# Performance work log

Measured on AMD Instinct MI355X. Metric: run time of the kernel, lower is better.

Reference implementation:

```python
import jax, jax.numpy as jnp
import numpy as np
import math

B, L, D = 2, 2048, 512
H, HD = 8, 64                      # num_heads, head_dim = D // H
NG = D * (D - 1) // 2              # SO(D) generator count = 130816


def setup_inputs() -> dict:
    key = jax.random.key(0)
    ks = jax.random.split(key, 8)
    x = jax.random.normal(ks[0], (B, L, D), jnp.float32)
    # additive causal mask [L, L]
    mask = jnp.where(jnp.tril(jnp.ones((L, L), bool)), 0.0, -1e9).astype(jnp.float32)
    coef = lambda k: jax.random.normal(k, (NG,), jnp.float32) * 0.1
    basis = lambda k: jax.random.normal(k, (HD, HD), jnp.float32) * 0.1
    return {
        "x": x, "mask": mask,
        "coef_q": coef(ks[1]), "coef_k": coef(ks[2]),
        "coef_v": coef(ks[3]), "coef_o": coef(ks[4]),
        "bias_q": jnp.zeros((D,), jnp.float32), "bias_k": jnp.zeros((D,), jnp.float32),
        "bias_v": jnp.zeros((D,), jnp.float32), "bias_o": jnp.zeros((D,), jnp.float32),
        "basis_q": basis(ks[5]), "basis_k": basis(ks[6]),
    }


def _make_W(coefs):
    # W = I + sum_i coef_i * G_i, with G_i the antisymmetric basis (row-major i<j).
    iu = jnp.triu_indices(D, k=1)
    A = jnp.zeros((D, D), coefs.dtype).at[iu].set(coefs)
    return A - A.T + jnp.eye(D, dtype=coefs.dtype)


def _proj(x, coefs, bias):
    # F.linear(x, W, b) = x @ W.T + b
    return x @ _make_W(coefs).T + bias


def _invariants(t, basis):
    # t: [B, H, L, HD] -> concat(norm, t @ basis.T)[..., :HD]
    norm = jnp.linalg.norm(t, axis=-1, keepdims=True)
    ip = jnp.einsum('bhld,nd->bhln', t, basis)
    return jnp.concatenate([norm, ip], axis=-1)[..., :HD]


def reference(x, mask, coef_q, coef_k, coef_v, coef_o,
              bias_q, bias_k, bias_v, bias_o, basis_q, basis_k):
    split = lambda t: t.reshape(B, L, H, HD).transpose(0, 2, 1, 3)  # [B,H,L,HD]
    Q = split(_proj(x, coef_q, bias_q))
    K = split(_proj(x, coef_k, bias_k))
    V = split(_proj(x, coef_v, bias_v))
    Qi = _invariants(Q, basis_q)
    Ki = _invariants(K, basis_k)
    scores = jnp.einsum('bhld,bhmd->bhlm', Qi, Ki) / math.sqrt(HD) + mask
    attn = jax.nn.softmax(scores, axis=-1)
    out = jnp.einsum('bhlm,bhmd->bhld', attn, V)
    out = out.transpose(0, 2, 1, 3).reshape(B, L, D)
    return _proj(out, coef_o, bias_o)
```

## Files before the change

kernel.cpp:

```cpp
#include <hip/hip_runtime.h>
#include <hip/hip_bf16.h>
#include <math.h>

#define D_ 512
#define B_ 2
#define L_ 2048
#define H_ 8
#define HD_ 64

typedef __attribute__((ext_vector_type(8))) short short8;
typedef __attribute__((ext_vector_type(4))) float f32x4;
typedef _Float16 half8 __attribute__((ext_vector_type(8)));

__device__ __forceinline__ ushort f2bf(float f) {
  __hip_bfloat16 h = __float2bfloat16(f);
  return *(ushort*)&h;
}
__device__ __forceinline__ float bf2f(ushort u) {
  unsigned int v = ((unsigned int)u) << 16;
  union { unsigned int u; float f; } c; c.u = v; return c.f;
}
__device__ __forceinline__ ushort f2h(float f) {
  _Float16 h = (_Float16)f;
  return *(ushort*)&h;
}
__device__ __forceinline__ int swz(int row, int col) {
  return row*64 + (((col>>3) ^ (row&7))<<3) + (col&7);
}
__device__ __forceinline__ int tri_idx(int i, int j) {
  return i*(D_-1) - (i*(i-1))/2 + (j - i - 1);
}

#define GLL16(g, l) __builtin_amdgcn_global_load_lds( \
    (const __attribute__((address_space(1))) void*)(g), \
    (__attribute__((address_space(3))) void*)(l), 16, 0, 0)

__global__ void prep_kernel(const float* __restrict__ x,
                            const float* __restrict__ cq, const float* __restrict__ ck,
                            const float* __restrict__ cv, const float* __restrict__ co,
                            const float* __restrict__ basq, const float* __restrict__ bask,
                            ushort* __restrict__ xb, ushort* __restrict__ Wb,
                            ushort* __restrict__ Bq, ushort* __restrict__ Bk) {
  int blk = blockIdx.x, tid = threadIdx.x;
  if (blk < 2048) {
    int i = (blk*256 + tid)*4;
    float4 v = *(const float4*)(x + i);
    ushort4 o = make_ushort4(f2h(v.x), f2h(v.y), f2h(v.z), f2h(v.w));
    *(ushort4*)(xb + i) = o;
  } else if (blk < 6144) {
    int e = (blk-2048)*256 + tid;
    int m = e >> 18, n = (e>>9)&511, k = e&511;
    const float* cf = (m==0)?cq:(m==1)?ck:(m==2)?cv:co;
    float v = (k>n) ? cf[tri_idx(n,k)] : (k<n) ? -cf[tri_idx(k,n)] : 0.f;
    Wb[e] = f2h(v);
  } else {
    int e = (blk-6144)*256 + tid;
    int which = e >> 12, ee = e & 4095;
    int n = ee >> 6, d = ee & 63;
    const float* bs = which ? bask : basq;
    float v = (n==0) ? 0.f : bs[(n-1)*64 + d];
    (which ? Bk : Bq)[ee] = f2h(v);
  }
}

__global__ __launch_bounds__(256) void proj_kernel(
    const ushort* __restrict__ Xb, const float* __restrict__ Xf,
    const ushort* __restrict__ Wb,
    const float* __restrict__ bq, const float* __restrict__ bk,
    const float* __restrict__ bv, const float* __restrict__ bo,
    const ushort* __restrict__ Bq, const ushort* __restrict__ Bk,
    ushort* __restrict__ QiO, float* __restrict__ NqV,
    ushort* __restrict__ KiO, float* __restrict__ NkV,
    ushort* __restrict__ Vt_g, float* __restrict__ OutF,
    int mode_override)
{
  __shared__ ushort BufA[4096];
  __shared__ ushort BufB[4096];

  const int tid = threadIdx.x;
  const int lane = tid & 63, w = tid >> 6;
  const int lr = lane & 15, lg = lane >> 4;
  const int by = blockIdx.y;
  const int mode = (mode_override >= 0) ? mode_override : (by >> 6);
  const int mb   = (mode_override >= 0) ? by : (by & 63);
  const int h = blockIdx.x;
  const int n0 = h*64, m0 = mb*64;
  const ushort* Wm = Wb + (size_t)mode*262144;
  const float* bias = (mode==0)?bq:(mode==1)?bk:(mode==2)?bv:bo;

  f32x4 acc[4] = {};
  for (int k0 = 0; k0 < 512; k0 += 64) {
    __syncthreads();
    #pragma unroll
    for (int i = 0; i < 2; ++i) {
      int idx = tid + 256*i;
      int row = idx >> 3, c = idx & 7;
      if (Xb) {
        *(short8*)&BufA[swz(row, c*8)] = *(const short8*)(Xb + (size_t)(m0+row)*512 + k0 + c*8);
      } else {
        const float* s = Xf + (size_t)(m0+row)*512 + k0 + c*8;
        float4 a = *(const float4*)s, b2 = *(const float4*)(s+4);
        ushort u[8] = {f2h(a.x),f2h(a.y),f2h(a.z),f2h(a.w),
                       f2h(b2.x),f2h(b2.y),f2h(b2.z),f2h(b2.w)};
        *(short8*)&BufA[swz(row, c*8)] = *(short8*)u;
      }
      *(short8*)&BufB[swz(row, c*8)] = *(const short8*)(Wm + (size_t)(n0+row)*512 + k0 + c*8);
    }
    __syncthreads();
    half8 af[2];
    #pragma unroll
    for (int ks = 0; ks < 2; ++ks)
      af[ks] = *(const half8*)&BufA[swz(w*16+lr, (ks*4+lg)*8)];
    #pragma unroll
    for (int nb = 0; nb < 4; ++nb) {
      f32x4 a = acc[nb];
      #pragma unroll
      for (int ks = 0; ks < 2; ++ks) {
        half8 bfr = *(const half8*)&BufB[swz(nb*16+lr, (ks*4+lg)*8)];
        a = __builtin_amdgcn_mfma_f32_16x16x32_f16(af[ks], bfr, a, 0,0,0);
      }
      acc[nb] = a;
    }
  }

  float bias4[4];
  #pragma unroll
  for (int nb = 0; nb < 4; ++nb) bias4[nb] = bias[n0 + nb*16 + lr];
  float q[4][4];
  #pragma unroll
  for (int nb = 0; nb < 4; ++nb)
    #pragma unroll
    for (int r = 0; r < 4; ++r) {
      size_t m = m0 + w*16 + lg*4 + r;
      size_t idx = m*512 + n0 + nb*16 + lr;
      q[nb][r] = Xf[idx] + acc[nb][r] + bias4[nb];
    }

  if (mode == 2) {
    #pragma unroll
    for (int nb = 0; nb < 4; ++nb) {
      ushort4 o = make_ushort4(f2bf(q[nb][0]), f2bf(q[nb][1]), f2bf(q[nb][2]), f2bf(q[nb][3]));
      int b = m0 >> 11, l0 = (m0 & 2047) + w*16 + lg*4;
      size_t idx = (size_t)(b*8 + h)*131072 + (size_t)(nb*16 + lr)*2048 + l0;
      *(ushort4*)(Vt_g + idx) = o;
    }
    return;
  }
  if (mode == 3) {
    #pragma unroll
    for (int nb = 0; nb < 4; ++nb)
      #pragma unroll
      for (int r = 0; r < 4; ++r) {
        size_t m = m0 + w*16 + lg*4 + r;
        OutF[m*512 + n0 + nb*16 + lr] = q[nb][r];
      }
    return;
  }

  const float scale = (mode == 0) ? 0.125f : 1.0f;
  float norm[4];
  #pragma unroll
  for (int r = 0; r < 4; ++r) {
    float s = 0.f;
    #pragma unroll
    for (int nb = 0; nb < 4; ++nb) s = fmaf(q[nb][r], q[nb][r], s);
    s += __shfl_xor(s, 1, 16);
    s += __shfl_xor(s, 2, 16);
    s += __shfl_xor(s, 4, 16);
    s += __shfl_xor(s, 8, 16);
    norm[r] = sqrtf(s);
  }
  __syncthreads();
  {
    const ushort* Bsrc = (mode==0) ? Bq : Bk;
    #pragma unroll
    for (int i = 0; i < 2; ++i) {
      int idx = tid + 256*i;
      int row = idx >> 3, c = idx & 7;
      *(short8*)&BufB[swz(row, c*8)] = *(const short8*)(Bsrc + row*64 + c*8);
    }
  }
  #pragma unroll
  for (int nb = 0; nb < 4; ++nb)
    #pragma unroll
    for (int r = 0; r < 4; ++r)
      BufA[swz(w*16 + lg*4 + r, nb*16 + lr)] = f2h(q[nb][r]);
  __syncthreads();

  f32x4 acc2[4] = {};
  half8 af2[2];
  #pragma unroll
  for (int ks = 0; ks < 2; ++ks)
    af2[ks] = *(const half8*)&BufA[swz(w*16+lr, (ks*4+lg)*8)];
  #pragma unroll
  for (int nb = 0; nb < 4; ++nb) {
    f32x4 a = acc2[nb];
    #pragma unroll
    for (int ks = 0; ks < 2; ++ks) {
      half8 bfr = *(const half8*)&BufB[swz(nb*16+lr, (ks*4+lg)*8)];
      a = __builtin_amdgcn_mfma_f32_16x16x32_f16(af2[ks], bfr, a, 0,0,0);
    }
    acc2[nb] = a;
  }

  ushort* dst = (mode==0) ? QiO : KiO;
  float*  Nd  = (mode==0) ? NqV : NkV;
  int b = m0 >> 11;
  float rn[4] = {0.f, 0.f, 0.f, 0.f};
  #pragma unroll
  for (int nb = 0; nb < 4; ++nb)
    #pragma unroll
    for (int r = 0; r < 4; ++r) {
      int ninv = nb*16 + lr;
      int l = (m0 & 2047) + w*16 + lg*4 + r;
      float v = (ninv == 0) ? norm[r] : acc2[nb][r];
      v *= scale;
      rn[r] = fmaf(v, v, rn[r]);
      dst[((size_t)(b*8 + h)*2048 + l)*64 + ninv] = f2h(v);
    }
  #pragma unroll
  for (int r = 0; r < 4; ++r) {
    float s = rn[r];
    s += __shfl_xor(s, 1, 16);
    s += __shfl_xor(s, 2, 16);
    s += __shfl_xor(s, 4, 16);
    s += __shfl_xor(s, 8, 16);
    if (lr == 0) {
      int l = (m0 & 2047) + w*16 + lg*4 + r;
      Nd[(size_t)(b*8 + h)*2048 + l] = sqrtf(s);
    }
  }
}

__device__ __forceinline__ void stage_kv(const ushort* __restrict__ Kg,
                                         const ushort* __restrict__ Vg,
                                         ushort* KB, ushort* VB,
                                         int w, int lane) {
  const int r8 = lane >> 3;
  const int cx = (lane & 7) ^ r8;
  #pragma unroll
  for (int s = 0; s < 2; ++s) {
    const int seg = w*2 + s;
    const int row = seg*8 + r8;
    GLL16(Kg + (size_t)row*64 + cx*8,   (char*)KB + seg*1024);
    GLL16(Vg + (size_t)row*2048 + cx*8, (char*)VB + seg*1024);
  }
}

__global__ __launch_bounds__(256) void attn_kernel(
    const ushort* __restrict__ Qi_g, const float* __restrict__ NqV,
    const ushort* __restrict__ Ki_g, const float* __restrict__ NkV,
    const ushort* __restrict__ Vt_g,
    float* __restrict__ PartO, float* __restrict__ PartL)
{
  __shared__ ushort KS[2][4096], VS[2][4096], Pl[4096];

  const int tid = threadIdx.x;
  const int lane = tid & 63, w = tid >> 6;
  const int lr = lane & 15, lg = lane >> 4;
  const int blk = blockIdx.x;
  const int half = blk >> 9;
  const int rem = blk & 511;
  const int g  = rem >> 4;
  const int bh = rem & 15;
  const int qb = (g < 16) ? (31 - g) : (g - 16);
  const int T = qb + 1, mid = (T + 1) >> 1;
  const int lo = half ? mid : 0, hi = half ? T : mid;
  const ushort* Kg0 = Ki_g + (size_t)bh*131072;
  const ushort* Vg0 = Vt_g + (size_t)bh*131072;
  const float*  NkVg = NkV + (size_t)bh*2048;
  const int qg0 = qb*64;
  const int qloc = w*16 + lr;
  const int prow = qloc;

  const size_t qoff = ((size_t)bh*2048 + qg0 + qloc)*64;
  const half8 qf0 = *(const half8*)(Qi_g + qoff + lg*8);
  const half8 qf1 = *(const half8*)(Qi_g + qoff + 32 + lg*8);
  const float nqv = NqV[(size_t)bh*2048 + qg0 + qloc];

  float mk = -1e30f;
  for (int jj = lane; jj < T*64; jj += 64) mk = fmaxf(mk, NkVg[jj]);
  #pragma unroll
  for (int off = 1; off < 64; off <<= 1) mk = fmaxf(mk, __shfl_xor(mk, off));
  const float m_ub = nqv * mk;

  float l_lane = 0.f;
  f32x4 accO[4] = {};

  if (lo < hi)
    stage_kv(Kg0 + (size_t)lo*4096, Vg0 + lo*64, KS[lo&1], VS[lo&1], w, lane);

  for (int jb = lo; jb < hi; ++jb) {
    const int cur = jb & 1;
    if (jb + 1 < hi) {
      stage_kv(Kg0 + (size_t)(jb+1)*4096, Vg0 + (jb+1)*64,
               KS[cur^1], VS[cur^1], w, lane);
      asm volatile("s_waitcnt vmcnt(4)" ::: "memory");
    } else {
      asm volatile("s_waitcnt vmcnt(0)" ::: "memory");
    }
    __builtin_amdgcn_sched_barrier(0);
    __builtin_amdgcn_s_barrier();
    __builtin_amdgcn_sched_barrier(0);

    f32x4 sf[4];
    __builtin_amdgcn_s_setprio(1);
    #pragma unroll
    for (int cb = 0; cb < 4; ++cb) {
      f32x4 a = {0.f,0.f,0.f,0.f};
      half8 k0 = *(const half8*)&KS[cur][swz(cb*16+lr, lg*8)];
      half8 k1 = *(const half8*)&KS[cur][swz(cb*16+lr, (4+lg)*8)];
      a = __builtin_amdgcn_mfma_f32_16x16x32_f16(k0, qf0, a, 0,0,0);
      a = __builtin_amdgcn_mfma_f32_16x16x32_f16(k1, qf1, a, 0,0,0);
      sf[cb] = a;
    }
    __builtin_amdgcn_s_setprio(0);
    if (jb == qb) {
      #pragma unroll
      for (int cb = 0; cb < 4; ++cb)
        #pragma unroll
        for (int r = 0; r < 4; ++r)
          if (cb*16 + lg*4 + r > qloc) sf[cb][r] = -1e30f;
    }

    #pragma unroll
    for (int cb = 0; cb < 4; ++cb)
      #pragma unroll
      for (int r = 0; r < 4; ++r) {
        float p = __expf(sf[cb][r] - m_ub);
        l_lane += p;
        sf[cb][r] = p;
      }
    #pragma unroll
    for (int cb = 0; cb < 4; ++cb) {
      ushort4 pk = make_ushort4(f2bf(sf[cb][0]), f2bf(sf[cb][1]),
                                f2bf(sf[cb][2]), f2bf(sf[cb][3]));
      *(ushort4*)&Pl[swz(prow, cb*16 + lg*4)] = pk;
    }

    short8 pfr[2];
    #pragma unroll
    for (int ks = 0; ks < 2; ++ks)
      pfr[ks] = *(const short8*)&Pl[swz(prow, (ks*4+lg)*8)];
    __builtin_amdgcn_s_setprio(1);
    #pragma unroll
    for (int db = 0; db < 4; ++db) {
      f32x4 a = accO[db];
      short8 v0 = *(const short8*)&VS[cur][swz(db*16+lr, lg*8)];
      short8 v1 = *(const short8*)&VS[cur][swz(db*16+lr, (4+lg)*8)];
      a = __builtin_amdgcn_mfma_f32_16x16x32_bf16(v0, pfr[0], a, 0,0,0);
      a = __builtin_amdgcn_mfma_f32_16x16x32_bf16(v1, pfr[1], a, 0,0,0);
      accO[db] = a;
    }
    __builtin_amdgcn_s_setprio(0);

    __builtin_amdgcn_sched_barrier(0);
    __builtin_amdgcn_s_barrier();
    __builtin_amdgcn_sched_barrier(0);
  }

  l_lane += __shfl_xor(l_lane, 16);
  l_lane += __shfl_xor(l_lane, 32);
  const int pbase = half*512 + bh*32 + qb;
  #pragma unroll
  for (int db = 0; db < 4; ++db)
    *(f32x4*)(PartO + (size_t)pbase*4096 + qloc*64 + db*16 + lg*4) = accO[db];
  if (lg == 0) PartL[pbase*64 + qloc] = l_lane;
}

__global__ __launch_bounds__(256) void combine_kernel(
    const float* __restrict__ PartO, const float* __restrict__ PartL,
    float* __restrict__ AO)
{
  __shared__ float invL[64];
  const int blk = blockIdx.x;
  const int bh = blk >> 5, qb = blk & 31;
  const int b = bh >> 3, h = bh & 7;
  const int tid = threadIdx.x;
  if (tid < 64) {
    float l0 = PartL[(bh*32 + qb)*64 + tid];
    float l1 = PartL[(512 + bh*32 + qb)*64 + tid];
    invL[tid] = 1.0f / (l0 + l1);
  }
  __syncthreads();
  const size_t base0 = (size_t)(bh*32 + qb)*4096;
  const size_t base1 = base0 + (size_t)512*4096;
  for (int t = tid; t < 1024; t += 256) {
    int idx = t*4, row = idx >> 6, col = idx & 63;
    float4 a = *(const float4*)(PartO + base0 + idx);
    float4 c = *(const float4*)(PartO + base1 + idx);
    float s = invL[row];
    float4 o = make_float4((a.x+c.x)*s, (a.y+c.y)*s, (a.z+c.z)*s, (a.w+c.w)*s);
    *(float4*)(AO + ((size_t)(b*2048 + qb*64 + row))*512 + h*64 + col) = o;
  }
}

extern "C" void kernel_launch(void* const* d_in, const int* in_sizes, int n_in,
                              void* d_out, int out_size, void* d_ws, size_t ws_size,
                              hipStream_t stream) {
  const float* x       = (const float*)d_in[0];
  const float* coef_q  = (const float*)d_in[2];
  const float* coef_k  = (const float*)d_in[3];
  const float* coef_v  = (const float*)d_in[4];
  const float* coef_o  = (const float*)d_in[5];
  const float* bias_q  = (const float*)d_in[6];
  const float* bias_k  = (const float*)d_in[7];
  const float* bias_v  = (const float*)d_in[8];
  const float* bias_o  = (const float*)d_in[9];
  const float* basis_q = (const float*)d_in[10];
  const float* basis_k = (const float*)d_in[11];
  float* out = (float*)d_out;

  ushort* xb    = (ushort*)d_ws;
  ushort* Wb    = xb + 2097152;
  ushort* Bq    = Wb + 1048576;
  ushort* Bk    = Bq + 4096;
  ushort* Qi    = Bk + 4096;
  ushort* Ki    = Qi + 2097152;
  ushort* Vt_g  = Ki + 2097152;
  float*  AO    = (float*)(Vt_g + 2097152);
  float*  NqV   = AO + 2097152;
  float*  NkV   = NqV + 32768;
  float*  PartO = NkV + 32768;
  float*  PartL = PartO + 4194304;

  prep_kernel<<<dim3(6176), 256, 0, stream>>>(x, coef_q, coef_k, coef_v, coef_o,
                                              basis_q, basis_k, xb, Wb, Bq, Bk);

  proj_kernel<<<dim3(8, 192), 256, 0, stream>>>(xb, x, Wb,
      bias_q, bias_k, bias_v, bias_o, Bq, Bk,
      Qi, NqV, Ki, NkV, Vt_g, nullptr, -1);

  attn_kernel<<<dim3(1024), 256, 0, stream>>>(Qi, NqV, Ki, NkV, Vt_g,
                                              PartO, PartL);

  combine_kernel<<<dim3(512), 256, 0, stream>>>(PartO, PartL, AO);

  proj_kernel<<<dim3(8, 64), 256, 0, stream>>>(nullptr, AO, Wb,
      bias_q, bias_k, bias_v, bias_o, Bq, Bk,
      Qi, NqV, Ki, NkV, Vt_g, out, 3);
}
```

Baseline: 92.52 us.

## Fuse QKV projections into one kernel and fold combine into output projection

The three Q/K/V projection modes now run in one kernel that loads each X tile once and multiplies it against all three weight tiles, so the grid shrinks from 192 to 64 row blocks. The split-K combine step is folded into the output projection, which normalizes the partial outputs while staging its A tile and keeps the exact fp32 values for the residual in shared memory. This removes the AO round trip and one launch. The setprio hints in the attention kernel are also removed. The trade-offs are fewer blocks, so lower parallelism, and more shared memory and registers per block. Each output projection block also recomputes the combine for all heads, reading PartO redundantly across the 8 column blocks.

```diff
diff --git a/kernel.cpp b/kernel.cpp
--- a/kernel.cpp
+++ b/kernel.cpp
@@ -63,48 +63,42 @@
   }
 }
 
-__global__ __launch_bounds__(256) void proj_kernel(
+__global__ __launch_bounds__(256) void proj_qkv_kernel(
     const ushort* __restrict__ Xb, const float* __restrict__ Xf,
     const ushort* __restrict__ Wb,
     const float* __restrict__ bq, const float* __restrict__ bk,
-    const float* __restrict__ bv, const float* __restrict__ bo,
+    const float* __restrict__ bv,
     const ushort* __restrict__ Bq, const ushort* __restrict__ Bk,
     ushort* __restrict__ QiO, float* __restrict__ NqV,
     ushort* __restrict__ KiO, float* __restrict__ NkV,
-    ushort* __restrict__ Vt_g, float* __restrict__ OutF,
-    int mode_override)
+    ushort* __restrict__ Vt_g)
 {
   __shared__ ushort BufA[4096];
-  __shared__ ushort BufB[4096];
+  __shared__ ushort BufQ[4096];
+  __shared__ ushort BufK[4096];
+  __shared__ ushort BufV[4096];
 
   const int tid = threadIdx.x;
   const int lane = tid & 63, w = tid >> 6;
   const int lr = lane & 15, lg = lane >> 4;
-  const int by = blockIdx.y;
-  const int mode = (mode_override >= 0) ? mode_override : (by >> 6);
-  const int mb   = (mode_override >= 0) ? by : (by & 63);
-  const int h = blockIdx.x;
+  const int h = blockIdx.x, mb = blockIdx.y;
   const int n0 = h*64, m0 = mb*64;
-  const ushort* Wm = Wb + (size_t)mode*262144;
-  const float* bias = (mode==0)?bq:(mode==1)?bk:(mode==2)?bv:bo;
-
-  f32x4 acc[4] = {};
+  const ushort* Wq = Wb;
+  const ushort* Wk = Wb + 262144;
+  const ushort* Wv = Wb + 524288;
+
+  f32x4 accQ[4] = {}, accK[4] = {}, accV[4] = {};
   for (int k0 = 0; k0 < 512; k0 += 64) {
     __syncthreads();
     #pragma unroll
     for (int i = 0; i < 2; ++i) {
       int idx = tid + 256*i;
       int row = idx >> 3, c = idx & 7;
-      if (Xb) {
-        *(short8*)&BufA[swz(row, c*8)] = *(const short8*)(Xb + (size_t)(m0+row)*512 + k0 + c*8);
-      } else {
-        const float* s = Xf + (size_t)(m0+row)*512 + k0 + c*8;
-        float4 a = *(const float4*)s, b2 = *(const float4*)(s+4);
-        ushort u[8] = {f2h(a.x),f2h(a.y),f2h(a.z),f2h(a.w),
-                       f2h(b2.x),f2h(b2.y),f2h(b2.z),f2h(b2.w)};
-        *(short8*)&BufA[swz(row, c*8)] = *(short8*)u;
-      }
-      *(short8*)&BufB[swz(row, c*8)] = *(const short8*)(Wm + (size_t)(n0+row)*512 + k0 + c*8);
+      int so = swz(row, c*8);
+      *(short8*)&BufA[so] = *(const short8*)(Xb + (size_t)(m0+row)*512 + k0 + c*8);
+      *(short8*)&BufQ[so] = *(const short8*)(Wq + (size_t)(n0+row)*512 + k0 + c*8);
+      *(short8*)&BufK[so] = *(const short8*)(Wk + (size_t)(n0+row)*512 + k0 + c*8);
+      *(short8*)&BufV[so] = *(const short8*)(Wv + (size_t)(n0+row)*512 + k0 + c*8);
     }
     __syncthreads();
     half8 af[2];
@@ -113,121 +107,129 @@
       af[ks] = *(const half8*)&BufA[swz(w*16+lr, (ks*4+lg)*8)];
     #pragma unroll
     for (int nb = 0; nb < 4; ++nb) {
-      f32x4 a = acc[nb];
       #pragma unroll
       for (int ks = 0; ks < 2; ++ks) {
-        half8 bfr = *(const half8*)&BufB[swz(nb*16+lr, (ks*4+lg)*8)];
-        a = __builtin_amdgcn_mfma_f32_16x16x32_f16(af[ks], bfr, a, 0,0,0);
+        int so = swz(nb*16+lr, (ks*4+lg)*8);
+        accQ[nb] = __builtin_amdgcn_mfma_f32_16x16x32_f16(af[ks], *(const half8*)&BufQ[so], accQ[nb], 0,0,0);
+        accK[nb] = __builtin_amdgcn_mfma_f32_16x16x32_f16(af[ks], *(const half8*)&BufK[so], accK[nb], 0,0,0);
+        accV[nb] = __builtin_amdgcn_mfma_f32_16x16x32_f16(af[ks], *(const half8*)&BufV[so], accV[nb], 0,0,0);
       }
-      acc[nb] = a;
-    }
-  }
-
-  float bias4[4];
-  #pragma unroll
-  for (int nb = 0; nb < 4; ++nb) bias4[nb] = bias[n0 + nb*16 + lr];
-  float q[4][4];
+    }
+  }
+
+  float ex[4][4];
   #pragma unroll
   for (int nb = 0; nb < 4; ++nb)
     #pragma unroll
     for (int r = 0; r < 4; ++r) {
       size_t m = m0 + w*16 + lg*4 + r;
-      size_t idx = m*512 + n0 + nb*16 + lr;
-      q[nb][r] = Xf[idx] + acc[nb][r] + bias4[nb];
-    }
-
-  if (mode == 2) {
+      ex[nb][r] = Xf[m*512 + n0 + nb*16 + lr];
+    }
+  const int b = m0 >> 11;
+
+  #pragma unroll
+  for (int nb = 0; nb < 4; ++nb) {
+    float bv4 = bv[n0 + nb*16 + lr];
+    float v0 = ex[nb][0] + accV[nb][0] + bv4;
+    float v1 = ex[nb][1] + accV[nb][1] + bv4;
+    float v2 = ex[nb][2] + accV[nb][2] + bv4;
+    float v3 = ex[nb][3] + accV[nb][3] + bv4;
+    ushort4 o = make_ushort4(f2bf(v0), f2bf(v1), f2bf(v2), f2bf(v3));
+    int l0 = (m0 & 2047) + w*16 + lg*4;
+    size_t idx = (size_t)(b*8 + h)*131072 + (size_t)(nb*16 + lr)*2048 + l0;
+    *(ushort4*)(Vt_g + idx) = o;
+  }
+
+  float qQ[4][4], qK[4][4];
+  #pragma unroll
+  for (int nb = 0; nb < 4; ++nb) {
+    float bq4 = bq[n0 + nb*16 + lr];
+    float bk4 = bk[n0 + nb*16 + lr];
+    #pragma unroll
+    for (int r = 0; r < 4; ++r) {
+      qQ[nb][r] = ex[nb][r] + accQ[nb][r] + bq4;
+      qK[nb][r] = ex[nb][r] + accK[nb][r] + bk4;
+    }
+  }
+  float normQ[4], normK[4];
+  #pragma unroll
+  for (int r = 0; r < 4; ++r) {
+    float sq = 0.f, sk = 0.f;
     #pragma unroll
     for (int nb = 0; nb < 4; ++nb) {
-      ushort4 o = make_ushort4(f2bf(q[nb][0]), f2bf(q[nb][1]), f2bf(q[nb][2]), f2bf(q[nb][3]));
-      int b = m0 >> 11, l0 = (m0 & 2047) + w*16 + lg*4;
-      size_t idx = (size_t)(b*8 + h)*131072 + (size_t)(nb*16 + lr)*2048 + l0;
-      *(ushort4*)(Vt_g + idx) = o;
-    }
-    return;
-  }
-  if (mode == 3) {
-    #pragma unroll
-    for (int nb = 0; nb < 4; ++nb)
-      #pragma unroll
-      for (int r = 0; r < 4; ++r) {
-        size_t m = m0 + w*16 + lg*4 + r;
-        OutF[m*512 + n0 + nb*16 + lr] = q[nb][r];
-      }
-    return;
-  }
-
-  const float scale = (mode == 0) ? 0.125f : 1.0f;
-  float norm[4];
-  #pragma unroll
-  for (int r = 0; r < 4; ++r) {
-    float s = 0.f;
-    #pragma unroll
-    for (int nb = 0; nb < 4; ++nb) s = fmaf(q[nb][r], q[nb][r], s);
-    s += __shfl_xor(s, 1, 16);
-    s += __shfl_xor(s, 2, 16);
-    s += __shfl_xor(s, 4, 16);
-    s += __shfl_xor(s, 8, 16);
-    norm[r] = sqrtf(s);
+      sq = fmaf(qQ[nb][r], qQ[nb][r], sq);
+      sk = fmaf(qK[nb][r], qK[nb][r], sk);
+    }
+    sq += __shfl_xor(sq, 1, 16); sk += __shfl_xor(sk, 1, 16);
+    sq += __shfl_xor(sq, 2, 16); sk += __shfl_xor(sk, 2, 16);
+    sq += __shfl_xor(sq, 4, 16); sk += __shfl_xor(sk, 4, 16);
+    sq += __shfl_xor(sq, 8, 16); sk += __shfl_xor(sk, 8, 16);
+    normQ[r] = sqrtf(sq); normK[r] = sqrtf(sk);
   }
   __syncthreads();
   {
-    const ushort* Bsrc = (mode==0) ? Bq : Bk;
     #pragma unroll
     for (int i = 0; i < 2; ++i) {
       int idx = tid + 256*i;
       int row = idx >> 3, c = idx & 7;
-      *(short8*)&BufB[swz(row, c*8)] = *(const short8*)(Bsrc + row*64 + c*8);
+      int so = swz(row, c*8);
+      *(short8*)&BufQ[so] = *(const short8*)(Bq + row*64 + c*8);
+      *(short8*)&BufK[so] = *(const short8*)(Bk + row*64 + c*8);
     }
   }
   #pragma unroll
   for (int nb = 0; nb < 4; ++nb)
     #pragma unroll
-    for (int r = 0; r < 4; ++r)
-      BufA[swz(w*16 + lg*4 + r, nb*16 + lr)] = f2h(q[nb][r]);
+    for (int r = 0; r < 4; ++r) {
+      int so = swz(w*16 + lg*4 + r, nb*16 + lr);
+      BufA[so] = f2h(qQ[nb][r]);
+      BufV[so] = f2h(qK[nb][r]);
+    }
   __syncthreads();
 
-  f32x4 acc2[4] = {};
-  half8 af2[2];
-  #pragma unroll
-  for (int ks = 0; ks < 2; ++ks)
-    af2[ks] = *(const half8*)&BufA[swz(w*16+lr, (ks*4+lg)*8)];
+  f32x4 acc2Q[4] = {}, acc2K[4] = {};
+  half8 aq[2], ak[2];
+  #pragma unroll
+  for (int ks = 0; ks < 2; ++ks) {
+    aq[ks] = *(const half8*)&BufA[swz(w*16+lr, (ks*4+lg)*8)];
+    ak[ks] = *(const half8*)&BufV[swz(w*16+lr, (ks*4+lg)*8)];
+  }
   #pragma unroll
   for (int nb = 0; nb < 4; ++nb) {
-    f32x4 a = acc2[nb];
     #pragma unroll
     for (int ks = 0; ks < 2; ++ks) {
-      half8 bfr = *(const half8*)&BufB[swz(nb*16+lr, (ks*4+lg)*8)];
-      a = __builtin_amdgcn_mfma_f32_16x16x32_f16(af2[ks], bfr, a, 0,0,0);
-    }
-    acc2[nb] = a;
-  }
-
-  ushort* dst = (mode==0) ? QiO : KiO;
-  float*  Nd  = (mode==0) ? NqV : NkV;
-  int b = m0 >> 11;
-  float rn[4] = {0.f, 0.f, 0.f, 0.f};
+      int so = swz(nb*16+lr, (ks*4+lg)*8);
+      acc2Q[nb] = __builtin_amdgcn_mfma_f32_16x16x32_f16(aq[ks], *(const half8*)&BufQ[so], acc2Q[nb], 0,0,0);
+      acc2K[nb] = __builtin_amdgcn_mfma_f32_16x16x32_f16(ak[ks], *(const half8*)&BufK[so], acc2K[nb], 0,0,0);
+    }
+  }
+
+  float rnq[4] = {0.f,0.f,0.f,0.f}, rnk[4] = {0.f,0.f,0.f,0.f};
   #pragma unroll
   for (int nb = 0; nb < 4; ++nb)
     #pragma unroll
     for (int r = 0; r < 4; ++r) {
       int ninv = nb*16 + lr;
       int l = (m0 & 2047) + w*16 + lg*4 + r;
-      float v = (ninv == 0) ? norm[r] : acc2[nb][r];
-      v *= scale;
-      rn[r] = fmaf(v, v, rn[r]);
-      dst[((size_t)(b*8 + h)*2048 + l)*64 + ninv] = f2h(v);
+      float vq = (ninv == 0) ? normQ[r] : acc2Q[nb][r];
+      vq *= 0.125f;
+      rnq[r] = fmaf(vq, vq, rnq[r]);
+      QiO[((size_t)(b*8 + h)*2048 + l)*64 + ninv] = f2h(vq);
+      float vk = (ninv == 0) ? normK[r] : acc2K[nb][r];
+      rnk[r] = fmaf(vk, vk, rnk[r]);
+      KiO[((size_t)(b*8 + h)*2048 + l)*64 + ninv] = f2h(vk);
     }
   #pragma unroll
   for (int r = 0; r < 4; ++r) {
-    float s = rn[r];
-    s += __shfl_xor(s, 1, 16);
-    s += __shfl_xor(s, 2, 16);
-    s += __shfl_xor(s, 4, 16);
-    s += __shfl_xor(s, 8, 16);
+    float sq = rnq[r], sk = rnk[r];
+    sq += __shfl_xor(sq, 1, 16); sk += __shfl_xor(sk, 1, 16);
+    sq += __shfl_xor(sq, 2, 16); sk += __shfl_xor(sk, 2, 16);
+    sq += __shfl_xor(sq, 4, 16); sk += __shfl_xor(sk, 4, 16);
+    sq += __shfl_xor(sq, 8, 16); sk += __shfl_xor(sk, 8, 16);
     if (lr == 0) {
       int l = (m0 & 2047) + w*16 + lg*4 + r;
-      Nd[(size_t)(b*8 + h)*2048 + l] = sqrtf(s);
+      NqV[(size_t)(b*8 + h)*2048 + l] = sqrtf(sq);
+      NkV[(size_t)(b*8 + h)*2048 + l] = sqrtf(sk);
     }
   }
 }
@@ -304,7 +306,6 @@
     __builtin_amdgcn_sched_barrier(0);
 
     f32x4 sf[4];
-    __builtin_amdgcn_s_setprio(1);
     #pragma unroll
     for (int cb = 0; cb < 4; ++cb) {
       f32x4 a = {0.f,0.f,0.f,0.f};
@@ -314,7 +315,6 @@
       a = __builtin_amdgcn_mfma_f32_16x16x32_f16(k1, qf1, a, 0,0,0);
       sf[cb] = a;
     }
-    __builtin_amdgcn_s_setprio(0);
     if (jb == qb) {
       #pragma unroll
       for (int cb = 0; cb < 4; ++cb)
@@ -342,7 +342,6 @@
     #pragma unroll
     for (int ks = 0; ks < 2; ++ks)
       pfr[ks] = *(const short8*)&Pl[swz(prow, (ks*4+lg)*8)];
-    __builtin_amdgcn_s_setprio(1);
     #pragma unroll
     for (int db = 0; db < 4; ++db) {
       f32x4 a = accO[db];
@@ -352,7 +351,6 @@
       a = __builtin_amdgcn_mfma_f32_16x16x32_bf16(v1, pfr[1], a, 0,0,0);
       accO[db] = a;
     }
-    __builtin_amdgcn_s_setprio(0);
 
     __builtin_amdgcn_sched_barrier(0);
     __builtin_amdgcn_s_barrier();
@@ -368,30 +366,78 @@
   if (lg == 0) PartL[pbase*64 + qloc] = l_lane;
 }
 
-__global__ __launch_bounds__(256) void combine_kernel(
+__global__ __launch_bounds__(256) void proj_o_kernel(
     const float* __restrict__ PartO, const float* __restrict__ PartL,
-    float* __restrict__ AO)
+    const ushort* __restrict__ Wb, const float* __restrict__ bo,
+    float* __restrict__ OutF)
 {
-  __shared__ float invL[64];
-  const int blk = blockIdx.x;
-  const int bh = blk >> 5, qb = blk & 31;
-  const int b = bh >> 3, h = bh & 7;
+  __shared__ ushort BufA[4096];
+  __shared__ ushort BufB[4096];
+  __shared__ float ExactT[64][65];
+
   const int tid = threadIdx.x;
-  if (tid < 64) {
-    float l0 = PartL[(bh*32 + qb)*64 + tid];
-    float l1 = PartL[(512 + bh*32 + qb)*64 + tid];
-    invL[tid] = 1.0f / (l0 + l1);
-  }
-  __syncthreads();
-  const size_t base0 = (size_t)(bh*32 + qb)*4096;
-  const size_t base1 = base0 + (size_t)512*4096;
-  for (int t = tid; t < 1024; t += 256) {
-    int idx = t*4, row = idx >> 6, col = idx & 63;
-    float4 a = *(const float4*)(PartO + base0 + idx);
-    float4 c = *(const float4*)(PartO + base1 + idx);
-    float s = invL[row];
-    float4 o = make_float4((a.x+c.x)*s, (a.y+c.y)*s, (a.z+c.z)*s, (a.w+c.w)*s);
-    *(float4*)(AO + ((size_t)(b*2048 + qb*64 + row))*512 + h*64 + col) = o;
+  const int lane = tid & 63, w = tid >> 6;
+  const int lr = lane & 15, lg = lane >> 4;
+  const int h = blockIdx.x, mb = blockIdx.y;
+  const int n0 = h*64, m0 = mb*64;
+  const ushort* Wm = Wb + 3*262144;
+  const int b_ = m0 >> 11;
+  const int qb_ = (m0 & 2047) >> 6;
+
+  f32x4 acc[4] = {};
+  for (int k0 = 0; k0 < 512; k0 += 64) {
+    __syncthreads();
+    const int hh = k0 >> 6;
+    const int bh_ = b_*8 + hh;
+    const size_t pb0 = (size_t)(bh_*32 + qb_)*4096;
+    const int lbase = (bh_*32 + qb_)*64;
+    #pragma unroll
+    for (int i = 0; i < 2; ++i) {
+      int idx = tid + 256*i;
+      int row = idx >> 3, c = idx & 7;
+      float l0 = PartL[lbase + row];
+      float l1 = PartL[32768 + lbase + row];
+      float inv = 1.0f / (l0 + l1);
+      const float* s0 = PartO + pb0 + row*64 + c*8;
+      const float* s1 = s0 + 2097152;
+      float4 a0 = *(const float4*)s0, a1 = *(const float4*)(s0+4);
+      float4 c0 = *(const float4*)s1, c1 = *(const float4*)(s1+4);
+      float o[8] = {(a0.x+c0.x)*inv, (a0.y+c0.y)*inv, (a0.z+c0.z)*inv, (a0.w+c0.w)*inv,
+                    (a1.x+c1.x)*inv, (a1.y+c1.y)*inv, (a1.z+c1.z)*inv, (a1.w+c1.w)*inv};
+      if (hh == h) {
+        #pragma unroll
+        for (int k = 0; k < 8; ++k) ExactT[row][c*8+k] = o[k];
+      }
+      ushort u[8];
+      #pragma unroll
+      for (int k = 0; k < 8; ++k) u[k] = f2h(o[k]);
+      *(short8*)&BufA[swz(row, c*8)] = *(short8*)u;
+      *(short8*)&BufB[swz(row, c*8)] = *(const short8*)(Wm + (size_t)(n0+row)*512 + k0 + c*8);
+    }
+    __syncthreads();
+    half8 af[2];
+    #pragma unroll
+    for (int ks = 0; ks < 2; ++ks)
+      af[ks] = *(const half8*)&BufA[swz(w*16+lr, (ks*4+lg)*8)];
+    #pragma unroll
+    for (int nb = 0; nb < 4; ++nb) {
+      #pragma unroll
+      for (int ks = 0; ks < 2; ++ks) {
+        half8 bfr = *(const half8*)&BufB[swz(nb*16+lr, (ks*4+lg)*8)];
+        acc[nb] = __builtin_amdgcn_mfma_f32_16x16x32_f16(af[ks], bfr, acc[nb], 0,0,0);
+      }
+    }
+  }
+
+  #pragma unroll
+  for (int nb = 0; nb < 4; ++nb) {
+    float bo4 = bo[n0 + nb*16 + lr];
+    #pragma unroll
+    for (int r = 0; r < 4; ++r) {
+      int row = w*16 + lg*4 + r;
+      size_t m = m0 + row;
+      OutF[m*512 + n0 + nb*16 + lr] = ExactT[row][nb*16 + lr] + acc[nb][r] + bo4;
+    }
   }
 }
 
@@ -418,8 +464,7 @@
   ushort* Qi    = Bk + 4096;
   ushort* Ki    = Qi + 2097152;
   ushort* Vt_g  = Ki + 2097152;
-  float*  AO    = (float*)(Vt_g + 2097152);
-  float*  NqV   = AO + 2097152;
+  float*  NqV   = (float*)(Vt_g + 2097152);
   float*  NkV   = NqV + 32768;
   float*  PartO = NkV + 32768;
   float*  PartL = PartO + 4194304;
@@ -427,16 +472,11 @@
   prep_kernel<<<dim3(6176), 256, 0, stream>>>(x, coef_q, coef_k, coef_v, coef_o,
                                               basis_q, basis_k, xb, Wb, Bq, Bk);
 
-  proj_kernel<<<dim3(8, 192), 256, 0, stream>>>(xb, x, Wb,
-      bias_q, bias_k, bias_v, bias_o, Bq, Bk,
-      Qi, NqV, Ki, NkV, Vt_g, nullptr, -1);
+  proj_qkv_kernel<<<dim3(8, 64), 256, 0, stream>>>(xb, x, Wb,
+      bias_q, bias_k, bias_v, Bq, Bk, Qi, NqV, Ki, NkV, Vt_g);
 
   attn_kernel<<<dim3(1024), 256, 0, stream>>>(Qi, NqV, Ki, NkV, Vt_g,
                                               PartO, PartL);
 
-  combine_kernel<<<dim3(512), 256, 0, stream>>>(PartO, PartL, AO);
-
-  proj_kernel<<<dim3(8, 64), 256, 0, stream>>>(nullptr, AO, Wb,
-      bias_q, bias_k, bias_v, bias_o, Bq, Bk,
-      Qi, NqV, Ki, NkV, Vt_g, out, 3);
-}
+  proj_o_kernel<<<dim3(8, 64), 256, 0, stream>>>(PartO, PartL, Wb, bias_o, out);
+}
```

Result: faster. 82.85 us (-10.5%).
